# Kernel tuning notes

Measured on AMD Instinct MI355X. Metric: run time of the kernel, lower is better.

## Reference

```python
import jax, jax.numpy as jnp
import numpy as np

B, T, N, S = 32, 64, 2048, 2048
DEMB = DENC = DDEC = 256


def setup_inputs() -> dict:
    key = jax.random.key(0)
    ks = jax.random.split(key, 14)
    u = lambda k, shp, s=0.05: jax.random.uniform(k, shp, jnp.float32, -s, s)
    return {
        "emb": jax.random.normal(ks[0], (B, N, DEMB), jnp.float32),
        "emb_mask": jnp.ones((B, N), jnp.float32),
        "enc": jax.random.normal(ks[1], (B, S, DENC), jnp.float32),
        "enc_mask": jnp.ones((B, S), jnp.float32),
        "gt": jax.random.randint(ks[2], (B, T), 0, N),
        "go": jax.random.uniform(ks[3], (DEMB,), jnp.float32, -0.1, 0.1),
        "Wih": u(ks[4], (4 * DDEC, DEMB)),
        "Whh": u(ks[5], (4 * DDEC, DDEC)),
        "bih": u(ks[6], (4 * DDEC,)),
        "bhh": u(ks[7], (4 * DDEC,)),
        "Wdt": u(ks[8], (DENC, DDEC)),
        "bdt": u(ks[9], (DENC,)),
        "Wf": u(ks[10], (DEMB + 1, DENC + DDEC)),
        "bf": u(ks[11], (DEMB + 1,)),
    }


def _pointer_decode(emb, emb_mask, enc, enc_mask, gt, go, Wih, Whh, bih, bhh, Wdt, bdt, Wf, bf):
    b, n, demb = emb.shape
    t = gt.shape[1]
    h = Whh.shape[1]
    # picked_t at step t is the (clipped) one-hot sum of gt[:, :t] (exclusive)
    onehot = jax.nn.one_hot(gt, n, dtype=emb.dtype)              # [B,T,N]
    picked = jnp.clip(jnp.cumsum(onehot, axis=1) - onehot, 0.0, 1.0)
    # teacher-forced LSTM inputs: go at t=0, then emb gathered at gt[:, t-1]
    prev = jnp.take_along_axis(emb, gt[:, :-1, None], axis=1)    # [B,T-1,demb]
    x = jnp.concatenate([jnp.broadcast_to(go, (b, 1, demb)), prev], axis=1)

    def cell(carry, x_t):
        h_t, c_t = carry
        g = x_t @ Wih.T + bih + h_t @ Whh.T + bhh                # [B,4H]
        i, f, gg, o = jnp.split(g, 4, axis=-1)                   # torch gate order i,f,g,o
        c_new = jax.nn.sigmoid(f) * c_t + jax.nn.sigmoid(i) * jnp.tanh(gg)
        h_new = jax.nn.sigmoid(o) * jnp.tanh(c_new)
        return (h_new, c_new), h_new

    h0 = jnp.zeros((b, h), emb.dtype)
    _, hs = jax.lax.scan(cell, (h0, h0), jnp.swapaxes(x, 0, 1))
    hs = jnp.swapaxes(hs, 0, 1)                                  # [B,T,H]
    # DotAttn: project dec state to denc, masked softmax over enc positions
    dec = hs @ Wdt.T + bdt                                       # [B,T,denc]
    raw = jnp.einsum('btd,bsd->bts', dec, enc)
    raw = raw - (1.0 - enc_mask)[:, None, :] * 1e20
    w = jax.nn.softmax(raw, axis=-1)
    attn = jnp.einsum('bts,bsd->btd', w, enc)                    # [B,T,denc]
    feat = jnp.concatenate([hs, attn], axis=-1) @ Wf.T + bf      # [B,T,demb+1]
    # pointer score: feat . concat([emb, picked]) over last dim, split to avoid [B,T,N,demb+1]
    score = jnp.einsum('btk,bnk->btn', feat[..., :demb], emb)
    score = score + feat[..., -1][:, :, None] * picked
    score = score - (1.0 - emb_mask)[:, None, :] * 1e20
    return score                                                 # [B,T,N]


def reference(emb, emb_mask, enc, enc_mask, gt, go, Wih, Whh, bih, bhh, Wdt, bdt, Wf, bf):
    return _pointer_decode(emb, emb_mask, enc, enc_mask, gt, go, Wih, Whh, bih, bhh, Wdt, bdt, Wf, bf)
```

## Files before the change

kernel.cpp:

```cpp
#include <hip/hip_runtime.h>
#include <cstddef>

#define BB 32
#define TT 64
#define NN_ 2048
#define SS 2048
#define DD 256
#define GG 1024
#define LP 32
#define FLD 264

typedef __attribute__((ext_vector_type(8))) short short8;
typedef __attribute__((ext_vector_type(4))) float f32x4;

static __device__ inline unsigned short f2bf(float f) {
    union { float f; unsigned int u; } v; v.f = f;
    unsigned int u = v.u;
    unsigned int r = u + 0x7FFF + ((u >> 16) & 1);
    return (unsigned short)(r >> 16);
}

static __device__ inline short8 pack8(float4 a, float4 b) {
    short8 s;
    s[0] = (short)f2bf(a.x); s[1] = (short)f2bf(a.y);
    s[2] = (short)f2bf(a.z); s[3] = (short)f2bf(a.w);
    s[4] = (short)f2bf(b.x); s[5] = (short)f2bf(b.y);
    s[6] = (short)f2bf(b.z); s[7] = (short)f2bf(b.w);
    return s;
}

static __device__ inline bool ok32(unsigned int v) {
    unsigned int x = v ^ 0x7F807F80u;
    return (((x - 0x00010001u) & ~x & 0x80008000u) == 0u);
}

__global__ __launch_bounds__(256) void k_prep(const int* __restrict__ gt,
                                              int* __restrict__ firstpos,
                                              unsigned int* __restrict__ hbuf32) {
    int T = blockIdx.x * 256 + threadIdx.x;
    int b = T >> 11, n = T & 2047;
    const int* g = gt + b * TT;
    int ft = TT;
#pragma unroll
    for (int t = 0; t < TT; ++t)
        if (g[t] == n && t < ft) ft = t;
    firstpos[T] = ft;
#pragma unroll
    for (int k = 0; k < 4; ++k)
        hbuf32[T + 65536 * k] = 0x7F807F80u;
}

__global__ __launch_bounds__(256) void gemm_xw(
        const float* __restrict__ emb, const int* __restrict__ gt,
        const float* __restrict__ go, const float* __restrict__ Wih,
        float* __restrict__ xW,
        const float* __restrict__ bih, const float* __restrict__ bhh) {
    int tm = blockIdx.y * 64, tn = blockIdx.x * 64;
    __shared__ short Ab[64][72];
    __shared__ short Bb[64][72];
    int tid = threadIdx.x, lane = tid & 63, wid = tid >> 6;
    int wm = wid & 1, wn = wid >> 1;
    f32x4 zero = {0.f, 0.f, 0.f, 0.f};
    f32x4 acc[2][2] = {{zero, zero}, {zero, zero}};
    int row = tid >> 2, kk = (tid & 3) * 16;
    int m = tm + row, b = m >> 6, t = m & 63;
    const float* arow = (t == 0) ? go
        : emb + ((size_t)b * NN_ + gt[b * TT + t - 1]) * DD;
    const float* ap = arow + kk;
    const float* bp = Wih + (size_t)(tn + row) * DD + kk;

    for (int k0 = 0; k0 < DD; k0 += 64) {
        float4 a0 = *(const float4*)(ap + k0);
        float4 a1 = *(const float4*)(ap + k0 + 4);
        float4 a2 = *(const float4*)(ap + k0 + 8);
        float4 a3 = *(const float4*)(ap + k0 + 12);
        float4 b0 = *(const float4*)(bp + k0);
        float4 b1 = *(const float4*)(bp + k0 + 4);
        float4 b2 = *(const float4*)(bp + k0 + 8);
        float4 b3 = *(const float4*)(bp + k0 + 12);
        *(short8*)&Ab[row][kk]     = pack8(a0, a1);
        *(short8*)&Ab[row][kk + 8] = pack8(a2, a3);
        *(short8*)&Bb[row][kk]     = pack8(b0, b1);
        *(short8*)&Bb[row][kk + 8] = pack8(b2, b3);
        __syncthreads();
#pragma unroll
        for (int kt = 0; kt < 2; ++kt) {
            int k8 = kt * 32 + (lane >> 4) * 8;
            short8 fa0 = *(const short8*)&Ab[wm * 32 + (lane & 15)][k8];
            short8 fa1 = *(const short8*)&Ab[wm * 32 + 16 + (lane & 15)][k8];
            short8 fb0 = *(const short8*)&Bb[wn * 32 + (lane & 15)][k8];
            short8 fb1 = *(const short8*)&Bb[wn * 32 + 16 + (lane & 15)][k8];
            acc[0][0] = __builtin_amdgcn_mfma_f32_16x16x32_bf16(fa0, fb0, acc[0][0], 0, 0, 0);
            acc[0][1] = __builtin_amdgcn_mfma_f32_16x16x32_bf16(fa0, fb1, acc[0][1], 0, 0, 0);
            acc[1][0] = __builtin_amdgcn_mfma_f32_16x16x32_bf16(fa1, fb0, acc[1][0], 0, 0, 0);
            acc[1][1] = __builtin_amdgcn_mfma_f32_16x16x32_bf16(fa1, fb1, acc[1][1], 0, 0, 0);
        }
        __syncthreads();
    }

#pragma unroll
    for (int i = 0; i < 2; ++i)
#pragma unroll
        for (int j = 0; j < 2; ++j)
#pragma unroll
            for (int r = 0; r < 4; ++r) {
                int lrow = wm * 32 + i * 16 + (lane >> 4) * 4 + r;
                int gcol = tn + wn * 32 + j * 16 + (lane & 15);
                xW[(size_t)(tm + lrow) * GG + gcol] =
                    acc[i][j][r] + bih[gcol] + bhh[gcol];
            }
}

__global__ __launch_bounds__(256) void gemm_bf16_nt(
        const float* __restrict__ A, const float* __restrict__ Bm,
        float* __restrict__ C, int K, int lda, int ldb, int ldc,
        long sA, long sB, long sC, int Nlim,
        const float* __restrict__ bias1,
        const int* __restrict__ firstpos, const float* __restrict__ emb_mask,
        int fscol) {
    int bz = blockIdx.z;
    A += (size_t)bz * sA; Bm += (size_t)bz * sB; C += (size_t)bz * sC;
    int tm = blockIdx.y * 64, tn = blockIdx.x * 64;
    __shared__ short Ab[64][72];
    __shared__ short Bb[64][72];
    __shared__ float sfs[64];
    int tid = threadIdx.x, lane = tid & 63, wid = tid >> 6;
    int wm = wid & 1, wn = wid >> 1;

    if (fscol >= 0 && tid < 64) sfs[tid] = A[(size_t)(tm + tid) * lda + fscol];

    f32x4 zero = {0.f, 0.f, 0.f, 0.f};
    f32x4 acc[2][2] = {{zero, zero}, {zero, zero}};

    int row = tid >> 2, kk = (tid & 3) * 16;
    int brow = tn + row; if (brow >= Nlim) brow = Nlim - 1;
    const float* ap = &A[(size_t)(tm + row) * lda + kk];
    const float* bp = &Bm[(size_t)brow * ldb + kk];

    for (int k0 = 0; k0 < K; k0 += 64) {
        float4 a0 = *(const float4*)(ap + k0);
        float4 a1 = *(const float4*)(ap + k0 + 4);
        float4 a2 = *(const float4*)(ap + k0 + 8);
        float4 a3 = *(const float4*)(ap + k0 + 12);
        float4 b0 = *(const float4*)(bp + k0);
        float4 b1 = *(const float4*)(bp + k0 + 4);
        float4 b2 = *(const float4*)(bp + k0 + 8);
        float4 b3 = *(const float4*)(bp + k0 + 12);
        *(short8*)&Ab[row][kk]     = pack8(a0, a1);
        *(short8*)&Ab[row][kk + 8] = pack8(a2, a3);
        *(short8*)&Bb[row][kk]     = pack8(b0, b1);
        *(short8*)&Bb[row][kk + 8] = pack8(b2, b3);
        __syncthreads();
#pragma unroll
        for (int kt = 0; kt < 2; ++kt) {
            int k8 = kt * 32 + (lane >> 4) * 8;
            short8 fa0 = *(const short8*)&Ab[wm * 32 + (lane & 15)][k8];
            short8 fa1 = *(const short8*)&Ab[wm * 32 + 16 + (lane & 15)][k8];
            short8 fb0 = *(const short8*)&Bb[wn * 32 + (lane & 15)][k8];
            short8 fb1 = *(const short8*)&Bb[wn * 32 + 16 + (lane & 15)][k8];
            acc[0][0] = __builtin_amdgcn_mfma_f32_16x16x32_bf16(fa0, fb0, acc[0][0], 0, 0, 0);
            acc[0][1] = __builtin_amdgcn_mfma_f32_16x16x32_bf16(fa0, fb1, acc[0][1], 0, 0, 0);
            acc[1][0] = __builtin_amdgcn_mfma_f32_16x16x32_bf16(fa1, fb0, acc[1][0], 0, 0, 0);
            acc[1][1] = __builtin_amdgcn_mfma_f32_16x16x32_bf16(fa1, fb1, acc[1][1], 0, 0, 0);
        }
        __syncthreads();
    }

#pragma unroll
    for (int i = 0; i < 2; ++i) {
#pragma unroll
        for (int j = 0; j < 2; ++j) {
#pragma unroll
            for (int r = 0; r < 4; ++r) {
                int lrow = wm * 32 + i * 16 + (lane >> 4) * 4 + r;
                int gcol = tn + wn * 32 + j * 16 + (lane & 15);
                if (gcol < Nlim) {
                    float v = acc[i][j][r];
                    if (bias1) v += bias1[gcol];
                    if (firstpos) {
                        int grow = tm + lrow;
                        if (firstpos[(size_t)bz * NN_ + gcol] < grow) v += sfs[lrow];
                        v -= (1.0f - emb_mask[(size_t)bz * NN_ + gcol]) * 1e20f;
                    }
                    C[(size_t)(tm + lrow) * ldc + gcol] = v;
                }
            }
        }
    }
}

__global__ __launch_bounds__(256) void gemm_dec(
        const unsigned int* __restrict__ hs16, const float* __restrict__ Wdt,
        float* __restrict__ dec, const float* __restrict__ bdt) {
    int tm = blockIdx.y * 64, tn = blockIdx.x * 64;
    __shared__ short Ab[64][72];
    __shared__ short Bb[64][72];
    int tid = threadIdx.x, lane = tid & 63, wid = tid >> 6;
    int wm = wid & 1, wn = wid >> 1;
    f32x4 zero = {0.f, 0.f, 0.f, 0.f};
    f32x4 acc[2][2] = {{zero, zero}, {zero, zero}};
    int row = tid >> 2, kk = (tid & 3) * 16;
    const short* ap16 = (const short*)hs16 + (size_t)(tm + row) * DD + kk;
    const float* bp = Wdt + (size_t)(tn + row) * DD + kk;

    for (int k0 = 0; k0 < DD; k0 += 64) {
        *(short8*)&Ab[row][kk]     = *(const short8*)(ap16 + k0);
        *(short8*)&Ab[row][kk + 8] = *(const short8*)(ap16 + k0 + 8);
        float4 b0 = *(const float4*)(bp + k0);
        float4 b1 = *(const float4*)(bp + k0 + 4);
        float4 b2 = *(const float4*)(bp + k0 + 8);
        float4 b3 = *(const float4*)(bp + k0 + 12);
        *(short8*)&Bb[row][kk]     = pack8(b0, b1);
        *(short8*)&Bb[row][kk + 8] = pack8(b2, b3);
        __syncthreads();
#pragma unroll
        for (int kt = 0; kt < 2; ++kt) {
            int k8 = kt * 32 + (lane >> 4) * 8;
            short8 fa0 = *(const short8*)&Ab[wm * 32 + (lane & 15)][k8];
            short8 fa1 = *(const short8*)&Ab[wm * 32 + 16 + (lane & 15)][k8];
            short8 fb0 = *(const short8*)&Bb[wn * 32 + (lane & 15)][k8];
            short8 fb1 = *(const short8*)&Bb[wn * 32 + 16 + (lane & 15)][k8];
            acc[0][0] = __builtin_amdgcn_mfma_f32_16x16x32_bf16(fa0, fb0, acc[0][0], 0, 0, 0);
            acc[0][1] = __builtin_amdgcn_mfma_f32_16x16x32_bf16(fa0, fb1, acc[0][1], 0, 0, 0);
            acc[1][0] = __builtin_amdgcn_mfma_f32_16x16x32_bf16(fa1, fb0, acc[1][0], 0, 0, 0);
            acc[1][1] = __builtin_amdgcn_mfma_f32_16x16x32_bf16(fa1, fb1, acc[1][1], 0, 0, 0);
        }
        __syncthreads();
    }

#pragma unroll
    for (int i = 0; i < 2; ++i)
#pragma unroll
        for (int j = 0; j < 2; ++j)
#pragma unroll
            for (int r = 0; r < 4; ++r) {
                int lrow = wm * 32 + i * 16 + (lane >> 4) * 4 + r;
                int gcol = tn + wn * 32 + j * 16 + (lane & 15);
                dec[(size_t)(tm + lrow) * DD + gcol] = acc[i][j][r] + bdt[gcol];
            }
}

__global__ __launch_bounds__(256) void gemm_feat(
        const unsigned int* __restrict__ hs16, const float* __restrict__ attn,
        const float* __restrict__ Wf, const float* __restrict__ bf,
        float* __restrict__ feat) {
    int tm = blockIdx.y * 64, tn = blockIdx.x * 64;
    __shared__ short Ab[64][72];
    __shared__ short Bb[64][72];
    int tid = threadIdx.x, lane = tid & 63, wid = tid >> 6;
    int wm = wid & 1, wn = wid >> 1;
    f32x4 zero = {0.f, 0.f, 0.f, 0.f};
    f32x4 acc[2][2] = {{zero, zero}, {zero, zero}};
    int row = tid >> 2, kk = (tid & 3) * 16;
    int brow = tn + row; if (brow > 256) brow = 256;
    const short* a16 = (const short*)hs16 + (size_t)(tm + row) * DD + kk;
    const float* af  = attn + (size_t)(tm + row) * DD + kk;
    const float* bp  = Wf + (size_t)brow * (2 * DD) + kk;

    for (int k0 = 0; k0 < 2 * DD; k0 += 64) {
        if (k0 < DD) {
            *(short8*)&Ab[row][kk]     = *(const short8*)(a16 + k0);
            *(short8*)&Ab[row][kk + 8] = *(const short8*)(a16 + k0 + 8);
        } else {
            float4 a0 = *(const float4*)(af + k0 - DD);
            float4 a1 = *(const float4*)(af + k0 - DD + 4);
            float4 a2 = *(const float4*)(af + k0 - DD + 8);
            float4 a3 = *(const float4*)(af + k0 - DD + 12);
            *(short8*)&Ab[row][kk]     = pack8(a0, a1);
            *(short8*)&Ab[row][kk + 8] = pack8(a2, a3);
        }
        float4 b0 = *(const float4*)(bp + k0);
        float4 b1 = *(const float4*)(bp + k0 + 4);
        float4 b2 = *(const float4*)(bp + k0 + 8);
        float4 b3 = *(const float4*)(bp + k0 + 12);
        *(short8*)&Bb[row][kk]     = pack8(b0, b1);
        *(short8*)&Bb[row][kk + 8] = pack8(b2, b3);
        __syncthreads();
#pragma unroll
        for (int kt = 0; kt < 2; ++kt) {
            int k8 = kt * 32 + (lane >> 4) * 8;
            short8 fa0 = *(const short8*)&Ab[wm * 32 + (lane & 15)][k8];
            short8 fa1 = *(const short8*)&Ab[wm * 32 + 16 + (lane & 15)][k8];
            short8 fb0 = *(const short8*)&Bb[wn * 32 + (lane & 15)][k8];
            short8 fb1 = *(const short8*)&Bb[wn * 32 + 16 + (lane & 15)][k8];
            acc[0][0] = __builtin_amdgcn_mfma_f32_16x16x32_bf16(fa0, fb0, acc[0][0], 0, 0, 0);
            acc[0][1] = __builtin_amdgcn_mfma_f32_16x16x32_bf16(fa0, fb1, acc[0][1], 0, 0, 0);
            acc[1][0] = __builtin_amdgcn_mfma_f32_16x16x32_bf16(fa1, fb0, acc[1][0], 0, 0, 0);
            acc[1][1] = __builtin_amdgcn_mfma_f32_16x16x32_bf16(fa1, fb1, acc[1][1], 0, 0, 0);
        }
        __syncthreads();
    }

#pragma unroll
    for (int i = 0; i < 2; ++i)
#pragma unroll
        for (int j = 0; j < 2; ++j)
#pragma unroll
            for (int r = 0; r < 4; ++r) {
                int lrow = wm * 32 + i * 16 + (lane >> 4) * 4 + r;
                int gcol = tn + wn * 32 + j * 16 + (lane & 15);
                if (gcol < DD + 1)
                    feat[(size_t)(tm + lrow) * FLD + gcol] = acc[i][j][r] + bf[gcol];
            }
}

__global__ __launch_bounds__(256) void k_flash(const float* __restrict__ dec,
                                               const float* __restrict__ enc,
                                               const float* __restrict__ enc_mask,
                                               float* __restrict__ part,
                                               float* __restrict__ lsum) {
    int c = blockIdx.x;
    int b = blockIdx.z;
    const float* Qf = dec + (size_t)b * TT * DD;
    const float* Eb = enc + (size_t)b * SS * DD;

    __shared__ short Vt[64][264];
    __shared__ short Pt[64][72];
    __shared__ float l_run[64][2];
    __shared__ float smsk[64];

    int tid = threadIdx.x, lane = tid & 63, wid = tid >> 6;
    int wm = wid & 1, wn = wid >> 1;
    int row = tid >> 2, kk = (tid & 3) * 16;

    short8 qf[8][2];
#pragma unroll
    for (int kt = 0; kt < 8; ++kt) {
        int kb = kt * 32 + (lane >> 4) * 8;
        const float* q0 = Qf + (size_t)(wm * 32 + (lane & 15)) * DD + kb;
        const float* q1 = Qf + (size_t)(wm * 32 + 16 + (lane & 15)) * DD + kb;
        qf[kt][0] = pack8(*(const float4*)q0, *(const float4*)(q0 + 4));
        qf[kt][1] = pack8(*(const float4*)q1, *(const float4*)(q1 + 4));
    }

    if (tid < 128) ((float*)l_run)[tid] = 0.0f;

    f32x4 zero = {0.f, 0.f, 0.f, 0.f};
    f32x4 aO[4][2][2];
#pragma unroll
    for (int dp = 0; dp < 4; ++dp)
#pragma unroll
        for (int i = 0; i < 2; ++i)
#pragma unroll
            for (int j = 0; j < 2; ++j) aO[dp][i][j] = zero;

    for (int kt64 = 0; kt64 < 4; ++kt64) {
        int s0 = c * 256 + kt64 * 64;
        __syncthreads();
#pragma unroll
        for (int kq = 0; kq < 4; ++kq) {
            const float* e = Eb + (size_t)(s0 + row) * DD + kq * 64 + kk;
            float4 e0 = *(const float4*)e;
            float4 e1 = *(const float4*)(e + 4);
            float4 e2 = *(const float4*)(e + 8);
            float4 e3 = *(const float4*)(e + 12);
            *(short8*)&Vt[row][kq * 64 + kk]     = pack8(e0, e1);
            *(short8*)&Vt[row][kq * 64 + kk + 8] = pack8(e2, e3);
        }
        if (tid < 64) smsk[tid] = enc_mask[(size_t)b * SS + s0 + tid];
        __syncthreads();

        f32x4 aS[2][2] = {{zero, zero}, {zero, zero}};
#pragma unroll
        for (int kt = 0; kt < 8; ++kt) {
            int k8 = kt * 32 + (lane >> 4) * 8;
            short8 fb0 = *(const short8*)&Vt[wn * 32 + (lane & 15)][k8];
            short8 fb1 = *(const short8*)&Vt[wn * 32 + 16 + (lane & 15)][k8];
            aS[0][0] = __builtin_amdgcn_mfma_f32_16x16x32_bf16(qf[kt][0], fb0, aS[0][0], 0, 0, 0);
            aS[0][1] = __builtin_amdgcn_mfma_f32_16x16x32_bf16(qf[kt][0], fb1, aS[0][1], 0, 0, 0);
            aS[1][0] = __builtin_amdgcn_mfma_f32_16x16x32_bf16(qf[kt][1], fb0, aS[1][0], 0, 0, 0);
            aS[1][1] = __builtin_amdgcn_mfma_f32_16x16x32_bf16(qf[kt][1], fb1, aS[1][1], 0, 0, 0);
        }

        int scol0 = wn * 32 + (lane & 15);
        float pen0 = (1.0f - smsk[scol0]) * 1e20f;
        float pen1 = (1.0f - smsk[scol0 + 16]) * 1e20f;
#pragma unroll
        for (int i = 0; i < 2; ++i)
#pragma unroll
            for (int r = 0; r < 4; ++r) {
                float p0 = __expf(aS[i][0][r] - pen0);
                float p1 = __expf(aS[i][1][r] - pen1);
                int trow = wm * 32 + i * 16 + (lane >> 4) * 4 + r;
                Pt[trow][scol0] = (short)f2bf(p0);
                Pt[trow][scol0 + 16] = (short)f2bf(p1);
                float rs = p0 + p1;
                rs += __shfl_xor(rs, 1);
                rs += __shfl_xor(rs, 2);
                rs += __shfl_xor(rs, 4);
                rs += __shfl_xor(rs, 8);
                if ((lane & 15) == 0) l_run[trow][wn] += rs;
            }
        __syncthreads();

#pragma unroll
        for (int kt = 0; kt < 2; ++kt) {
            int k8 = kt * 32 + (lane >> 4) * 8;
            short8 fa0 = *(const short8*)&Pt[wm * 32 + (lane & 15)][k8];
            short8 fa1 = *(const short8*)&Pt[wm * 32 + 16 + (lane & 15)][k8];
#pragma unroll
            for (int dp = 0; dp < 4; ++dp) {
                int dc = dp * 64 + wn * 32 + (lane & 15);
                short8 fb0, fb1;
#pragma unroll
                for (int e = 0; e < 8; ++e) {
                    fb0[e] = Vt[k8 + e][dc];
                    fb1[e] = Vt[k8 + e][dc + 16];
                }
                aO[dp][0][0] = __builtin_amdgcn_mfma_f32_16x16x32_bf16(fa0, fb0, aO[dp][0][0], 0, 0, 0);
                aO[dp][0][1] = __builtin_amdgcn_mfma_f32_16x16x32_bf16(fa0, fb1, aO[dp][0][1], 0, 0, 0);
                aO[dp][1][0] = __builtin_amdgcn_mfma_f32_16x16x32_bf16(fa1, fb0, aO[dp][1][0], 0, 0, 0);
                aO[dp][1][1] = __builtin_amdgcn_mfma_f32_16x16x32_bf16(fa1, fb1, aO[dp][1][1], 0, 0, 0);
            }
        }
    }
    __syncthreads();

    float* pp = part + ((size_t)(b * 8 + c) * 64) * 256;
#pragma unroll
    for (int dp = 0; dp < 4; ++dp)
#pragma unroll
        for (int i = 0; i < 2; ++i)
#pragma unroll
            for (int j = 0; j < 2; ++j)
#pragma unroll
                for (int r = 0; r < 4; ++r) {
                    int trow = wm * 32 + i * 16 + (lane >> 4) * 4 + r;
                    int dcol = dp * 64 + wn * 32 + j * 16 + (lane & 15);
                    pp[(size_t)trow * 256 + dcol] = aO[dp][i][j][r];
                }
    if (tid < 64)
        lsum[(size_t)(b * 8 + c) * 64 + tid] = l_run[tid][0] + l_run[tid][1];
}

__global__ __launch_bounds__(256) void k_amerge(const float* __restrict__ part,
                                                const float* __restrict__ lsum,
                                                float* __restrict__ attn) {
    int bt = blockIdx.x;
    int b = bt >> 6, t = bt & 63, d = threadIdx.x;
    float a = 0.0f, L = 0.0f;
#pragma unroll
    for (int c = 0; c < 8; ++c) {
        a += part[((size_t)(b * 8 + c) * 64 + t) * 256 + d];
        L += lsum[(size_t)(b * 8 + c) * 64 + t];
    }
    attn[(size_t)bt * 256 + d] = a / L;
}

__global__ __launch_bounds__(256) void k_lstm_mfma(const float* __restrict__ xW,
                                                   const float* __restrict__ Whh,
                                                   unsigned int* __restrict__ hbuf32,
                                                   unsigned int* __restrict__ hs16) {
    int p = blockIdx.x;
    int tid = threadIdx.x;
    int lane = tid & 63;
    int wid = tid >> 6;
    int mi = wid & 1;
    int ni = wid >> 1;
    int jj = lane >> 4;
    int bl = lane & 15;
    int j = p * 8 + mi * 4 + jj;
    int b = ni * 16 + bl;

    short8 afrag[8];
    {
        int rr = lane & 15;
        const float* wrow = Whh + (size_t)((rr & 3) * 256 + p * 8 + mi * 4 + (rr >> 2)) * DD;
#pragma unroll
        for (int kt = 0; kt < 8; ++kt) {
            short8 f;
#pragma unroll
            for (int e = 0; e < 8; ++e)
                f[e] = (short)f2bf(wrow[kt * 32 + (lane >> 4) * 8 + e]);
            afrag[kt] = f;
        }
    }

    float cstate = 0.0f;
    const int wb = jj * 128 + b;

    for (int t = 0; t < TT; ++t) {
        const float* g0 = xW + ((size_t)b * TT + t) * GG + j;
        float xb0 = g0[0], xb1 = g0[256], xb2 = g0[512], xb3 = g0[768];

        f32x4 acc = {0.f, 0.f, 0.f, 0.f};
        if (t > 0) {
            const unsigned int* hb = hbuf32 + (size_t)(t - 1) * 4096;
            unsigned int q[32];
            bool ready = false;
            while (!ready) {
                ready = true;
#pragma unroll
                for (int kt = 0; kt < 8; ++kt)
#pragma unroll
                    for (int w4 = 0; w4 < 4; ++w4)
                        q[kt * 4 + w4] = __hip_atomic_load(&hb[kt * 512 + wb + w4 * 32],
                            __ATOMIC_RELAXED, __HIP_MEMORY_SCOPE_AGENT);
#pragma unroll
                for (int i = 0; i < 32; ++i) ready = ready && ok32(q[i]);
            }
#pragma unroll
            for (int kt = 0; kt < 8; ++kt) {
                union { unsigned int w[4]; short8 s; } u;
                u.w[0] = q[kt * 4 + 0]; u.w[1] = q[kt * 4 + 1];
                u.w[2] = q[kt * 4 + 2]; u.w[3] = q[kt * 4 + 3];
                acc = __builtin_amdgcn_mfma_f32_16x16x32_bf16(afrag[kt], u.s, acc, 0, 0, 0);
            }
        }

        float pi = xb0 + acc[0];
        float pf = xb1 + acc[1];
        float pg = xb2 + acc[2];
        float po = xb3 + acc[3];
        float ig = 1.0f / (1.0f + __expf(-pi));
        float fg = 1.0f / (1.0f + __expf(-pf));
        float gg = tanhf(pg);
        float og = 1.0f / (1.0f + __expf(-po));
        cstate = fg * cstate + ig * gg;
        float hn = og * tanhf(cstate);

        float hnb = __shfl_down(hn, 16);
        if ((jj & 1) == 0) {
            unsigned int wv = (unsigned int)f2bf(hn) |
                              ((unsigned int)f2bf(hnb) << 16);
            int jp = p * 4 + mi * 2 + (jj >> 1);
            __hip_atomic_store(&hbuf32[(size_t)t * 4096 + jp * 32 + b],
                               wv, __ATOMIC_RELAXED, __HIP_MEMORY_SCOPE_AGENT);
            hs16[((size_t)b * TT + t) * 128 + jp] = wv;
        }
        asm volatile("s_waitcnt vmcnt(0)" ::: "memory");
    }
}

extern "C" void kernel_launch(void* const* d_in, const int* in_sizes, int n_in,
                              void* d_out, int out_size, void* d_ws, size_t ws_size,
                              hipStream_t stream) {
    const float* emb      = (const float*)d_in[0];
    const float* emb_mask = (const float*)d_in[1];
    const float* enc      = (const float*)d_in[2];
    const float* enc_mask = (const float*)d_in[3];
    const int*   gt       = (const int*)d_in[4];
    const float* go       = (const float*)d_in[5];
    const float* Wih      = (const float*)d_in[6];
    const float* Whh      = (const float*)d_in[7];
    const float* bih      = (const float*)d_in[8];
    const float* bhh      = (const float*)d_in[9];
    const float* Wdt      = (const float*)d_in[10];
    const float* bdt      = (const float*)d_in[11];
    const float* Wf       = (const float*)d_in[12];
    const float* bf       = (const float*)d_in[13];
    float* out = (float*)d_out;

    float* ws    = (float*)d_ws;
    float* xW    = ws;
    float* dec   = xW   + (size_t)BB * TT * GG;
    float* attn  = dec  + (size_t)BB * TT * DD;
    float* feat  = attn + (size_t)BB * TT * DD;
    float* part  = feat + (size_t)BB * TT * FLD;
    float* lsum  = part + (size_t)BB * 8 * TT * DD;
    int* firstpos = (int*)(lsum + (size_t)BB * 8 * TT);
    unsigned int* hbuf32 = (unsigned int*)(firstpos + (size_t)BB * NN_);
    unsigned int* hs16   = hbuf32 + (size_t)TT * 4096;

    k_prep<<<256, 256, 0, stream>>>(gt, firstpos, hbuf32);

    gemm_xw<<<dim3(GG / 64, BB * TT / 64, 1), 256, 0, stream>>>(
        emb, gt, go, Wih, xW, bih, bhh);

    k_lstm_mfma<<<LP, 256, 0, stream>>>(xW, Whh, hbuf32, hs16);

    gemm_dec<<<dim3(DD / 64, BB * TT / 64, 1), 256, 0, stream>>>(
        hs16, Wdt, dec, bdt);

    k_flash<<<dim3(8, 1, BB), 256, 0, stream>>>(dec, enc, enc_mask, part, lsum);
    k_amerge<<<BB * TT, 256, 0, stream>>>(part, lsum, attn);

    gemm_feat<<<dim3(5, BB * TT / 64, 1), 256, 0, stream>>>(
        hs16, attn, Wf, bf, feat);

    gemm_bf16_nt<<<dim3(NN_ / 64, 1, BB), 256, 0, stream>>>(
        feat, emb, out, DD, FLD, DD, NN_,
        (long)TT * FLD, (long)NN_ * DD, (long)TT * NN_, NN_,
        nullptr, firstpos, emb_mask, 256);
}
```

Baseline: 249.7 us.

## Fuse decoder projection GEMM into persistent LSTM kernel tail

Removes the separate gemm_dec launch and computes dec = hs·Wdtᵀ + bdt at the end of the persistent LSTM kernel. Each of the 32 blocks handles 64 rows and polls hs16, which is now pre-filled with a sentinel by k_prep, until the rows written by other blocks are complete. The goal is to drop a kernel launch and its tail gap. In exchange the GEMM runs on only 32 blocks, and the cross-block spin-polling on hs16 adds latency and depends on every block being co-resident.

```diff
diff --git a/kernel.cpp b/kernel.cpp
--- a/kernel.cpp
+++ b/kernel.cpp
@@ -34,6 +34,27 @@
     return (((x - 0x00010001u) & ~x & 0x80008000u) == 0u);
 }
 
+static __device__ inline unsigned long long ald64(const void* p) {
+    return __hip_atomic_load((const unsigned long long*)p, __ATOMIC_RELAXED,
+                             __HIP_MEMORY_SCOPE_AGENT);
+}
+
+static __device__ inline void poll8h(const unsigned int* p, unsigned int* q) {
+    for (;;) {
+        unsigned long long a0 = ald64(p),     a1 = ald64(p + 2);
+        unsigned long long a2 = ald64(p + 4), a3 = ald64(p + 6);
+        q[0] = (unsigned int)a0; q[1] = (unsigned int)(a0 >> 32);
+        q[2] = (unsigned int)a1; q[3] = (unsigned int)(a1 >> 32);
+        q[4] = (unsigned int)a2; q[5] = (unsigned int)(a2 >> 32);
+        q[6] = (unsigned int)a3; q[7] = (unsigned int)(a3 >> 32);
+        bool ok = true;
+#pragma unroll
+        for (int i = 0; i < 8; ++i) ok = ok && ok32(q[i]);
+        if (ok) return;
+        __builtin_amdgcn_s_sleep(16);
+    }
+}
+
 __global__ __launch_bounds__(256) void k_prep(const int* __restrict__ gt,
                                               int* __restrict__ firstpos,
                                               unsigned int* __restrict__ hbuf32) {
@@ -46,7 +67,7 @@
         if (g[t] == n && t < ft) ft = t;
     firstpos[T] = ft;
 #pragma unroll
-    for (int k = 0; k < 4; ++k)
+    for (int k = 0; k < 8; ++k)
         hbuf32[T + 65536 * k] = 0x7F807F80u;
 }
 
@@ -189,57 +210,6 @@
     }
 }
 
-__global__ __launch_bounds__(256) void gemm_dec(
-        const unsigned int* __restrict__ hs16, const float* __restrict__ Wdt,
-        float* __restrict__ dec, const float* __restrict__ bdt) {
-    int tm = blockIdx.y * 64, tn = blockIdx.x * 64;
-    __shared__ short Ab[64][72];
-    __shared__ short Bb[64][72];
-    int tid = threadIdx.x, lane = tid & 63, wid = tid >> 6;
-    int wm = wid & 1, wn = wid >> 1;
-    f32x4 zero = {0.f, 0.f, 0.f, 0.f};
-    f32x4 acc[2][2] = {{zero, zero}, {zero, zero}};
-    int row = tid >> 2, kk = (tid & 3) * 16;
-    const short* ap16 = (const short*)hs16 + (size_t)(tm + row) * DD + kk;
-    const float* bp = Wdt + (size_t)(tn + row) * DD + kk;
-
-    for (int k0 = 0; k0 < DD; k0 += 64) {
-        *(short8*)&Ab[row][kk]     = *(const short8*)(ap16 + k0);
-        *(short8*)&Ab[row][kk + 8] = *(const short8*)(ap16 + k0 + 8);
-        float4 b0 = *(const float4*)(bp + k0);
-        float4 b1 = *(const float4*)(bp + k0 + 4);
-        float4 b2 = *(const float4*)(bp + k0 + 8);
-        float4 b3 = *(const float4*)(bp + k0 + 12);
-        *(short8*)&Bb[row][kk]     = pack8(b0, b1);
-        *(short8*)&Bb[row][kk + 8] = pack8(b2, b3);
-        __syncthreads();
-#pragma unroll
-        for (int kt = 0; kt < 2; ++kt) {
-            int k8 = kt * 32 + (lane >> 4) * 8;
-            short8 fa0 = *(const short8*)&Ab[wm * 32 + (lane & 15)][k8];
-            short8 fa1 = *(const short8*)&Ab[wm * 32 + 16 + (lane & 15)][k8];
-            short8 fb0 = *(const short8*)&Bb[wn * 32 + (lane & 15)][k8];
-            short8 fb1 = *(const short8*)&Bb[wn * 32 + 16 + (lane & 15)][k8];
-            acc[0][0] = __builtin_amdgcn_mfma_f32_16x16x32_bf16(fa0, fb0, acc[0][0], 0, 0, 0);
-            acc[0][1] = __builtin_amdgcn_mfma_f32_16x16x32_bf16(fa0, fb1, acc[0][1], 0, 0, 0);
-            acc[1][0] = __builtin_amdgcn_mfma_f32_16x16x32_bf16(fa1, fb0, acc[1][0], 0, 0, 0);
-            acc[1][1] = __builtin_amdgcn_mfma_f32_16x16x32_bf16(fa1, fb1, acc[1][1], 0, 0, 0);
-        }
-        __syncthreads();
-    }
-
-#pragma unroll
-    for (int i = 0; i < 2; ++i)
-#pragma unroll
-        for (int j = 0; j < 2; ++j)
-#pragma unroll
-            for (int r = 0; r < 4; ++r) {
-                int lrow = wm * 32 + i * 16 + (lane >> 4) * 4 + r;
-                int gcol = tn + wn * 32 + j * 16 + (lane & 15);
-                dec[(size_t)(tm + lrow) * DD + gcol] = acc[i][j][r] + bdt[gcol];
-            }
-}
-
 __global__ __launch_bounds__(256) void gemm_feat(
         const unsigned int* __restrict__ hs16, const float* __restrict__ attn,
         const float* __restrict__ Wf, const float* __restrict__ bf,
@@ -450,7 +420,12 @@
 __global__ __launch_bounds__(256) void k_lstm_mfma(const float* __restrict__ xW,
                                                    const float* __restrict__ Whh,
                                                    unsigned int* __restrict__ hbuf32,
-                                                   unsigned int* __restrict__ hs16) {
+                                                   unsigned int* __restrict__ hs16,
+                                                   const float* __restrict__ Wdt,
+                                                   const float* __restrict__ bdt,
+                                                   float* __restrict__ dec) {
+    __shared__ short SA[64][72];
+    __shared__ short SB[64][72];
     int p = blockIdx.x;
     int tid = threadIdx.x;
     int lane = tid & 63;
@@ -478,12 +453,13 @@
 
     float cstate = 0.0f;
     const int wb = jj * 128 + b;
+    f32x4 zero = {0.f, 0.f, 0.f, 0.f};
 
     for (int t = 0; t < TT; ++t) {
         const float* g0 = xW + ((size_t)b * TT + t) * GG + j;
         float xb0 = g0[0], xb1 = g0[256], xb2 = g0[512], xb3 = g0[768];
 
-        f32x4 acc = {0.f, 0.f, 0.f, 0.f};
+        f32x4 acc = zero;
         if (t > 0) {
             const unsigned int* hb = hbuf32 + (size_t)(t - 1) * 4096;
             unsigned int q[32];
@@ -526,9 +502,61 @@
             int jp = p * 4 + mi * 2 + (jj >> 1);
             __hip_atomic_store(&hbuf32[(size_t)t * 4096 + jp * 32 + b],
                                wv, __ATOMIC_RELAXED, __HIP_MEMORY_SCOPE_AGENT);
-            hs16[((size_t)b * TT + t) * 128 + jp] = wv;
+            __hip_atomic_store(&hs16[((size_t)b * TT + t) * 128 + jp],
+                               wv, __ATOMIC_RELAXED, __HIP_MEMORY_SCOPE_AGENT);
         }
         asm volatile("s_waitcnt vmcnt(0)" ::: "memory");
+    }
+
+    {
+        int wm = wid & 1, wn = wid >> 1;
+        int row = tid >> 2, kk = (tid & 3) * 16;
+        int tm = p * 64;
+        const unsigned int* ah = hs16 + (size_t)(tm + row) * 128;
+        for (int n = 0; n < 4; ++n) {
+            int tn = n * 64;
+            f32x4 acc2[2][2] = {{zero, zero}, {zero, zero}};
+            const float* bp = Wdt + (size_t)(tn + row) * DD + kk;
+            for (int k0 = 0; k0 < DD; k0 += 64) {
+                unsigned int q[8];
+                poll8h(ah + ((k0 + kk) >> 1), q);
+                union { unsigned int u[8]; short8 s8[2]; } uu;
+#pragma unroll
+                for (int i = 0; i < 8; ++i) uu.u[i] = q[i];
+                *(short8*)&SA[row][kk]     = uu.s8[0];
+                *(short8*)&SA[row][kk + 8] = uu.s8[1];
+                float4 b0 = *(const float4*)(bp + k0);
+                float4 b1 = *(const float4*)(bp + k0 + 4);
+                float4 b2 = *(const float4*)(bp + k0 + 8);
+                float4 b3 = *(const float4*)(bp + k0 + 12);
+                *(short8*)&SB[row][kk]     = pack8(b0, b1);
+                *(short8*)&SB[row][kk + 8] = pack8(b2, b3);
+                __syncthreads();
+#pragma unroll
+                for (int kt = 0; kt < 2; ++kt) {
+                    int k8 = kt * 32 + (lane >> 4) * 8;
+                    short8 fa0 = *(const short8*)&SA[wm * 32 + (lane & 15)][k8];
+                    short8 fa1 = *(const short8*)&SA[wm * 32 + 16 + (lane & 15)][k8];
+                    short8 fb0 = *(const short8*)&SB[wn * 32 + (lane & 15)][k8];
+                    short8 fb1 = *(const short8*)&SB[wn * 32 + 16 + (lane & 15)][k8];
+                    acc2[0][0] = __builtin_amdgcn_mfma_f32_16x16x32_bf16(fa0, fb0, acc2[0][0], 0, 0, 0);
+                    acc2[0][1] = __builtin_amdgcn_mfma_f32_16x16x32_bf16(fa0, fb1, acc2[0][1], 0, 0, 0);
+                    acc2[1][0] = __builtin_amdgcn_mfma_f32_16x16x32_bf16(fa1, fb0, acc2[1][0], 0, 0, 0);
+                    acc2[1][1] = __builtin_amdgcn_mfma_f32_16x16x32_bf16(fa1, fb1, acc2[1][1], 0, 0, 0);
+                }
+                __syncthreads();
+            }
+#pragma unroll
+            for (int i = 0; i < 2; ++i)
+#pragma unroll
+                for (int jx = 0; jx < 2; ++jx)
+#pragma unroll
+                    for (int r = 0; r < 4; ++r) {
+                        int lrow = wm * 32 + i * 16 + (lane >> 4) * 4 + r;
+                        int gcol = tn + wn * 32 + jx * 16 + (lane & 15);
+                        dec[(size_t)(tm + lrow) * DD + gcol] = acc2[i][jx][r] + bdt[gcol];
+                    }
+        }
     }
 }
 
@@ -567,10 +595,7 @@
     gemm_xw<<<dim3(GG / 64, BB * TT / 64, 1), 256, 0, stream>>>(
         emb, gt, go, Wih, xW, bih, bhh);
 
-    k_lstm_mfma<<<LP, 256, 0, stream>>>(xW, Whh, hbuf32, hs16);
-
-    gemm_dec<<<dim3(DD / 64, BB * TT / 64, 1), 256, 0, stream>>>(
-        hs16, Wdt, dec, bdt);
+    k_lstm_mfma<<<LP, 256, 0, stream>>>(xW, Whh, hbuf32, hs16, Wdt, bdt, dec);
 
     k_flash<<<dim3(8, 1, BB), 256, 0, stream>>>(dec, enc, enc_mask, part, lsum);
     k_amerge<<<BB * TT, 256, 0, stream>>>(part, lsum, attn);
```

Measured after the change: 262.5 us. +5.1%, slower.
